# Optimization experiments

Hardware: AMD Instinct MI355X
Metric: run time of the kernel (lower is better)

## Reference

```python
import jax, jax.numpy as jnp
import numpy as np

TWO_PI = 6.283185  # constant used verbatim in the original module


def setup_inputs() -> dict:
    key = jax.random.key(0)
    ks = jax.random.split(key, 12)
    N, input_size, light_freq, H = 8388608, 11, 16, 16
    d_in = input_size - 2 + 2 * light_freq  # 41
    x = jax.random.uniform(ks[0], (N, input_size), dtype=jnp.float32)
    B_light = jax.random.normal(ks[1], (2, light_freq), dtype=jnp.float32)
    W1 = jax.random.normal(ks[2], (d_in, H), dtype=jnp.float32) * (1.0 / np.sqrt(d_in))
    b1 = jax.random.normal(ks[3], (H,), dtype=jnp.float32) * 0.01
    W2 = jax.random.normal(ks[4], (H, H), dtype=jnp.float32) * 0.25
    b2 = jax.random.normal(ks[5], (H,), dtype=jnp.float32) * 0.01
    W3 = jax.random.normal(ks[6], (H, H), dtype=jnp.float32) * 0.25
    b3 = jax.random.normal(ks[7], (H,), dtype=jnp.float32) * 0.01
    W4 = jax.random.normal(ks[8], (H, H), dtype=jnp.float32) * 0.25
    b4 = jax.random.normal(ks[9], (H,), dtype=jnp.float32) * 0.01
    W5 = jax.random.normal(ks[10], (H, 1), dtype=jnp.float32) * 0.25
    b5 = jax.random.normal(ks[11], (1,), dtype=jnp.float32) * 0.01
    return {"x": x, "B_light": B_light, "W1": W1, "b1": b1, "W2": W2, "b2": b2,
            "W3": W3, "b3": b3, "W4": W4, "b4": b4, "W5": W5, "b5": b5}


def reference(x, B_light, W1, b1, W2, b2, W3, b3, W4, b4, W5, b5):
    # Fourier-feature encoding of the last two input dims (light direction)
    x_light = TWO_PI * (x[:, -2:] @ B_light)                      # [N, F]
    feats = jnp.concatenate([x[:, :-2], jnp.cos(x_light), jnp.sin(x_light)], axis=-1)  # [N, 41]
    # Tiny 5-layer MLP with ELU activations
    h = jax.nn.elu(feats @ W1 + b1)
    h = jax.nn.elu(h @ W2 + b2)
    h = jax.nn.elu(h @ W3 + b3)
    h = jax.nn.elu(h @ W4 + b4)
    out = h @ W5 + b5                                             # [N, 1]
    return out
```

## Files before the change

kernel.cpp:

```cpp
#include <hip/hip_runtime.h>

typedef __fp16   cvt16x2 __attribute__((ext_vector_type(2)));
typedef _Float16 h2      __attribute__((ext_vector_type(2)));
typedef _Float16 half4_t __attribute__((ext_vector_type(4)));
typedef unsigned uint2v  __attribute__((ext_vector_type(2)));
typedef float    f32x4   __attribute__((ext_vector_type(4)));
typedef float    f32x4u  __attribute__((ext_vector_type(4), aligned(4)));

#define CH 8
#define LOG2E 1.44269504f
#define LN2   0.69314718f

#if !__has_builtin(__builtin_elementwise_exp2)
extern "C" __device__ _Float16 __ocml_exp2_f16(_Float16);
#endif

__device__ __forceinline__ unsigned pk(float a, float b) {
    cvt16x2 h = __builtin_amdgcn_cvt_pkrtz(a, b);
    return __builtin_bit_cast(unsigned, h);
}
__device__ __forceinline__ half4_t mkfrag(unsigned lo, unsigned hi) {
    uint2v u; u[0] = lo; u[1] = hi;
    return __builtin_bit_cast(half4_t, u);
}

__device__ __forceinline__ unsigned elu_pk(float a, float b) {
    h2 v = __builtin_bit_cast(h2, __builtin_amdgcn_cvt_pkrtz(a, b));
    const h2 z   = {(_Float16)0.f, (_Float16)0.f};
    const h2 lg  = {(_Float16)LOG2E, (_Float16)LOG2E};
    const h2 mlg = {(_Float16)(-LOG2E), (_Float16)(-LOG2E)};
    h2 t = __builtin_elementwise_min(v, z);
#if __has_builtin(__builtin_elementwise_exp2)
    h2 ev = __builtin_elementwise_exp2(t);
#else
    h2 ev; ev[0] = __ocml_exp2_f16(t[0]); ev[1] = __ocml_exp2_f16(t[1]);
#endif
    h2 r = __builtin_elementwise_max(v, ev * lg + mlg);
    return __builtin_bit_cast(unsigned, r);
}

__global__ __launch_bounds__(128, 4) void pixenc_mfma14(
    const float* __restrict__ x,
    const float* __restrict__ Bl,
    const float* __restrict__ W1, const float* __restrict__ b1,
    const float* __restrict__ W2, const float* __restrict__ b2,
    const float* __restrict__ W3, const float* __restrict__ b3,
    const float* __restrict__ W4, const float* __restrict__ b4,
    const float* __restrict__ W5, const float* __restrict__ b5,
    float* __restrict__ out)
{
    const int t    = threadIdx.x;
    const int lane = t & 63;
    const int w    = t >> 6;
    const int g    = lane >> 4;
    const int m    = lane & 15;

    const int coff = (g == 0) ? 7 : (g == 2) ? 3 : 0;

    half4_t A1[3], A2, A3, A4;
    #pragma unroll
    for (int e = 0; e < 4; ++e) {
        const bool valid = (g == 1) | (g == 0 && e < 2) | (g == 2 && e >= 1);
        A1[0][e] = valid ? (_Float16)(W1[(coff + e) * 16 + m] * LOG2E)
                         : (_Float16)0.f;
        A1[1][e] = (_Float16)(W1[(9  + g * 4 + e) * 16 + m] * LOG2E);
        A1[2][e] = (_Float16)(W1[(25 + g * 4 + e) * 16 + m] * LOG2E);
        A2[e]    = (_Float16)W2[(g * 4 + e) * 16 + m];
        A3[e]    = (_Float16)W3[(g * 4 + e) * 16 + m];
        A4[e]    = (_Float16)W4[(g * 4 + e) * 16 + m];
    }
    const half4_t Az = (g == 0) ? mkfrag(pk(Bl[m], Bl[16 + m]), 0u)
                                : mkfrag(0u, 0u);
    const half4_t A5 = (m == 0)
        ? mkfrag(pk(W5[g * 4 + 0] * LN2, W5[g * 4 + 1] * LN2),
                 pk(W5[g * 4 + 2] * LN2, W5[g * 4 + 3] * LN2))
        : mkfrag(0u, 0u);
    f32x4 c1, c2, c3, c4;
    #pragma unroll
    for (int e = 0; e < 4; ++e) {
        const int r = g * 4 + e;
        c1[e] = b1[r] * LOG2E; c2[e] = b2[r] * LOG2E;
        c3[e] = b3[r] * LOG2E; c4[e] = b4[r] * LOG2E;
    }
    const f32x4 zero4 = {0.f, 0.f, 0.f, 0.f};
    f32x4 c5 = zero4;
    if (g == 0) c5[0] = b5[0];

    const int wavebase = blockIdx.x * (128 * CH) + w * (64 * CH);
    const float* aP = x + (size_t)(wavebase + m) * 11 + coff;
    float* outp = out + wavebase + m;

    unsigned cp01[4], cp23[4];
    #pragma unroll
    for (int s = 0; s < 4; ++s) {
        const f32x4u v = *(const f32x4u*)(aP + s * 176);
        cp01[s] = pk(v[0], v[1]);
        cp23[s] = pk(v[2], v[3]);
    }

    #pragma unroll
    for (int c = 0; c < CH; ++c) {
        unsigned np01[4], np23[4];
        if (c + 1 < CH) {
            aP += 704;
            #pragma unroll
            for (int s = 0; s < 4; ++s) {
                const f32x4u v = *(const f32x4u*)(aP + s * 176);
                np01[s] = pk(v[0], v[1]);
                np23[s] = pk(v[2], v[3]);
            }
        }

        f32x4 az[4];
        #pragma unroll
        for (int s = 0; s < 4; ++s)
            az[s] = __builtin_amdgcn_mfma_f32_16x16x16f16(
                        Az, mkfrag(cp23[s], 0u), zero4, 0, 0, 0);

        f32x4 acc[4];
        #pragma unroll
        for (int s = 0; s < 4; ++s) {
            float cs[4], sn[4];
            #pragma unroll
            for (int e = 0; e < 4; ++e) {
                cs[e] = __builtin_amdgcn_cosf(az[s][e]);
                sn[e] = __builtin_amdgcn_sinf(az[s][e]);
            }
            const half4_t F0 = mkfrag(cp01[s], cp23[s]);
            const half4_t F1 = mkfrag(pk(cs[0], cs[1]), pk(cs[2], cs[3]));
            const half4_t F2 = mkfrag(pk(sn[0], sn[1]), pk(sn[2], sn[3]));
            f32x4 a = __builtin_amdgcn_mfma_f32_16x16x16f16(A1[0], F0, c1, 0, 0, 0);
            a = __builtin_amdgcn_mfma_f32_16x16x16f16(A1[1], F1, a, 0, 0, 0);
            a = __builtin_amdgcn_mfma_f32_16x16x16f16(A1[2], F2, a, 0, 0, 0);
            acc[s] = a;
        }

        half4_t H[4];
        #pragma unroll
        for (int s = 0; s < 4; ++s)
            H[s] = mkfrag(elu_pk(acc[s][0], acc[s][1]), elu_pk(acc[s][2], acc[s][3]));
        #pragma unroll
        for (int s = 0; s < 4; ++s)
            acc[s] = __builtin_amdgcn_mfma_f32_16x16x16f16(A2, H[s], c2, 0, 0, 0);

        #pragma unroll
        for (int s = 0; s < 4; ++s)
            H[s] = mkfrag(elu_pk(acc[s][0], acc[s][1]), elu_pk(acc[s][2], acc[s][3]));
        #pragma unroll
        for (int s = 0; s < 4; ++s)
            acc[s] = __builtin_amdgcn_mfma_f32_16x16x16f16(A3, H[s], c3, 0, 0, 0);

        #pragma unroll
        for (int s = 0; s < 4; ++s)
            H[s] = mkfrag(elu_pk(acc[s][0], acc[s][1]), elu_pk(acc[s][2], acc[s][3]));
        #pragma unroll
        for (int s = 0; s < 4; ++s)
            acc[s] = __builtin_amdgcn_mfma_f32_16x16x16f16(A4, H[s], c4, 0, 0, 0);

        #pragma unroll
        for (int s = 0; s < 4; ++s)
            H[s] = mkfrag(elu_pk(acc[s][0], acc[s][1]), elu_pk(acc[s][2], acc[s][3]));
        #pragma unroll
        for (int s = 0; s < 4; ++s) {
            const f32x4 oh = __builtin_amdgcn_mfma_f32_16x16x16f16(
                                 A5, H[s], c5, 0, 0, 0);
            if (g == 0) outp[c * 64 + s * 16] = oh[0];
        }

        if (c + 1 < CH) {
            #pragma unroll
            for (int s = 0; s < 4; ++s) {
                cp01[s] = np01[s]; cp23[s] = np23[s];
            }
        }
    }
}

__global__ void pixenc_tail(
    const float* __restrict__ x, const float* __restrict__ Bl,
    const float* __restrict__ W1, const float* __restrict__ b1,
    const float* __restrict__ W2, const float* __restrict__ b2,
    const float* __restrict__ W3, const float* __restrict__ b3,
    const float* __restrict__ W4, const float* __restrict__ b4,
    const float* __restrict__ W5, const float* __restrict__ b5,
    float* __restrict__ out, int N, int start)
{
    const int i = start + blockIdx.x * 256 + threadIdx.x;
    if (i >= N) return;
    const float* xr = x + (size_t)i * 11;
    float feats[41];
    for (int k = 0; k < 9; ++k) feats[k] = xr[k];
    for (int f = 0; f < 16; ++f) {
        const float ang = 6.283185f * (xr[9] * Bl[f] + xr[10] * Bl[16 + f]);
        float s, c; __sincosf(ang, &s, &c);
        feats[9 + f] = c; feats[25 + f] = s;
    }
    float h[16], gg[16];
    for (int j = 0; j < 16; ++j) h[j] = b1[j];
    for (int k = 0; k < 41; ++k)
        for (int j = 0; j < 16; ++j) h[j] = fmaf(feats[k], W1[k * 16 + j], h[j]);
    for (int j = 0; j < 16; ++j) h[j] = h[j] > 0.f ? h[j] : __expf(h[j]) - 1.f;
    for (int j = 0; j < 16; ++j) gg[j] = b2[j];
    for (int k = 0; k < 16; ++k)
        for (int j = 0; j < 16; ++j) gg[j] = fmaf(h[k], W2[k * 16 + j], gg[j]);
    for (int j = 0; j < 16; ++j) gg[j] = gg[j] > 0.f ? gg[j] : __expf(gg[j]) - 1.f;
    for (int j = 0; j < 16; ++j) h[j] = b3[j];
    for (int k = 0; k < 16; ++k)
        for (int j = 0; j < 16; ++j) h[j] = fmaf(gg[k], W3[k * 16 + j], h[j]);
    for (int j = 0; j < 16; ++j) h[j] = h[j] > 0.f ? h[j] : __expf(h[j]) - 1.f;
    for (int j = 0; j < 16; ++j) gg[j] = b4[j];
    for (int k = 0; k < 16; ++k)
        for (int j = 0; j < 16; ++j) gg[j] = fmaf(h[k], W4[k * 16 + j], gg[j]);
    for (int j = 0; j < 16; ++j) gg[j] = gg[j] > 0.f ? gg[j] : __expf(gg[j]) - 1.f;
    float o = b5[0];
    for (int j = 0; j < 16; ++j) o = fmaf(gg[j], W5[j], o);
    out[i] = o;
}

extern "C" void kernel_launch(void* const* d_in, const int* in_sizes, int n_in,
                              void* d_out, int out_size, void* d_ws, size_t ws_size,
                              hipStream_t stream) {
    const float* x  = (const float*)d_in[0];
    const float* Bl = (const float*)d_in[1];
    const float* W1 = (const float*)d_in[2];
    const float* b1 = (const float*)d_in[3];
    const float* W2 = (const float*)d_in[4];
    const float* b2 = (const float*)d_in[5];
    const float* W3 = (const float*)d_in[6];
    const float* b3 = (const float*)d_in[7];
    const float* W4 = (const float*)d_in[8];
    const float* b4 = (const float*)d_in[9];
    const float* W5 = (const float*)d_in[10];
    const float* b5 = (const float*)d_in[11];
    float* out = (float*)d_out;

    const int N = out_size;
    const int NB = N / (128 * CH);
    const int rem = N - NB * (128 * CH);
    if (NB > 0)
        pixenc_mfma14<<<NB, 128, 0, stream>>>(x, Bl, W1, b1, W2, b2, W3, b3,
                                              W4, b4, W5, b5, out);
    if (rem > 0)
        pixenc_tail<<<(rem + 255) / 256, 256, 0, stream>>>(
            x, Bl, W1, b1, W2, b2, W3, b3, W4, b4, W5, b5, out, N, NB * 128 * CH);
}
```

Before: 120.4 us.

## Process one 16-sample tile per iteration to cut registers and raise occupancy

Each wave now handles one 16-sample MFMA tile per loop iteration instead of four interleaved tiles, unrolled by two, with single-tile prefetch of the next input row. Launch bounds move to 8 waves per SIMD and the bias b5 is added as a scalar after the last MFMA. The aim is lower VGPR pressure and higher occupancy, hiding latency through more resident waves rather than instruction-level parallelism within a wave. The trade-off is less independent MFMA and transcendental work per wave to overlap dependent chains.

```diff
diff --git a/kernel.cpp b/kernel.cpp
--- a/kernel.cpp
+++ b/kernel.cpp
@@ -7,7 +7,7 @@
 typedef float    f32x4   __attribute__((ext_vector_type(4)));
 typedef float    f32x4u  __attribute__((ext_vector_type(4), aligned(4)));
 
-#define CH 8
+#define NSB 32
 #define LOG2E 1.44269504f
 #define LN2   0.69314718f
 
@@ -39,7 +39,7 @@
     return __builtin_bit_cast(unsigned, r);
 }
 
-__global__ __launch_bounds__(128, 4) void pixenc_mfma14(
+__global__ __launch_bounds__(128, 8) void pixenc_mfma17(
     const float* __restrict__ x,
     const float* __restrict__ Bl,
     const float* __restrict__ W1, const float* __restrict__ b1,
@@ -83,96 +83,55 @@
         c3[e] = b3[r] * LOG2E; c4[e] = b4[r] * LOG2E;
     }
     const f32x4 zero4 = {0.f, 0.f, 0.f, 0.f};
-    f32x4 c5 = zero4;
-    if (g == 0) c5[0] = b5[0];
-
-    const int wavebase = blockIdx.x * (128 * CH) + w * (64 * CH);
+    const float b5v = b5[0];
+
+    const int wavebase = blockIdx.x * (32 * NSB) + w * (16 * NSB);
     const float* aP = x + (size_t)(wavebase + m) * 11 + coff;
     float* outp = out + wavebase + m;
 
-    unsigned cp01[4], cp23[4];
-    #pragma unroll
-    for (int s = 0; s < 4; ++s) {
-        const f32x4u v = *(const f32x4u*)(aP + s * 176);
-        cp01[s] = pk(v[0], v[1]);
-        cp23[s] = pk(v[2], v[3]);
-    }
-
-    #pragma unroll
-    for (int c = 0; c < CH; ++c) {
-        unsigned np01[4], np23[4];
-        if (c + 1 < CH) {
-            aP += 704;
-            #pragma unroll
-            for (int s = 0; s < 4; ++s) {
-                const f32x4u v = *(const f32x4u*)(aP + s * 176);
-                np01[s] = pk(v[0], v[1]);
-                np23[s] = pk(v[2], v[3]);
-            }
+    unsigned cp01, cp23;
+    {
+        const f32x4u v = *(const f32x4u*)aP;
+        cp01 = pk(v[0], v[1]);
+        cp23 = pk(v[2], v[3]);
+    }
+
+    #pragma unroll 2
+    for (int it = 0; it < NSB; ++it) {
+        unsigned np01, np23;
+        if (it + 1 < NSB) {
+            const f32x4u v = *(const f32x4u*)(aP + 176);
+            np01 = pk(v[0], v[1]);
+            np23 = pk(v[2], v[3]);
         }
-
-        f32x4 az[4];
+        aP += 176;
+
+        const f32x4 az = __builtin_amdgcn_mfma_f32_16x16x16f16(
+                             Az, mkfrag(cp23, 0u), zero4, 0, 0, 0);
+        float cs[4], sn[4];
         #pragma unroll
-        for (int s = 0; s < 4; ++s)
-            az[s] = __builtin_amdgcn_mfma_f32_16x16x16f16(
-                        Az, mkfrag(cp23[s], 0u), zero4, 0, 0, 0);
-
-        f32x4 acc[4];
-        #pragma unroll
-        for (int s = 0; s < 4; ++s) {
-            float cs[4], sn[4];
-            #pragma unroll
-            for (int e = 0; e < 4; ++e) {
-                cs[e] = __builtin_amdgcn_cosf(az[s][e]);
-                sn[e] = __builtin_amdgcn_sinf(az[s][e]);
-            }
-            const half4_t F0 = mkfrag(cp01[s], cp23[s]);
-            const half4_t F1 = mkfrag(pk(cs[0], cs[1]), pk(cs[2], cs[3]));
-            const half4_t F2 = mkfrag(pk(sn[0], sn[1]), pk(sn[2], sn[3]));
-            f32x4 a = __builtin_amdgcn_mfma_f32_16x16x16f16(A1[0], F0, c1, 0, 0, 0);
-            a = __builtin_amdgcn_mfma_f32_16x16x16f16(A1[1], F1, a, 0, 0, 0);
-            a = __builtin_amdgcn_mfma_f32_16x16x16f16(A1[2], F2, a, 0, 0, 0);
-            acc[s] = a;
+        for (int e = 0; e < 4; ++e) {
+            cs[e] = __builtin_amdgcn_cosf(az[e]);
+            sn[e] = __builtin_amdgcn_sinf(az[e]);
         }
-
-        half4_t H[4];
-        #pragma unroll
-        for (int s = 0; s < 4; ++s)
-            H[s] = mkfrag(elu_pk(acc[s][0], acc[s][1]), elu_pk(acc[s][2], acc[s][3]));
-        #pragma unroll
-        for (int s = 0; s < 4; ++s)
-            acc[s] = __builtin_amdgcn_mfma_f32_16x16x16f16(A2, H[s], c2, 0, 0, 0);
-
-        #pragma unroll
-        for (int s = 0; s < 4; ++s)
-            H[s] = mkfrag(elu_pk(acc[s][0], acc[s][1]), elu_pk(acc[s][2], acc[s][3]));
-        #pragma unroll
-        for (int s = 0; s < 4; ++s)
-            acc[s] = __builtin_amdgcn_mfma_f32_16x16x16f16(A3, H[s], c3, 0, 0, 0);
-
-        #pragma unroll
-        for (int s = 0; s < 4; ++s)
-            H[s] = mkfrag(elu_pk(acc[s][0], acc[s][1]), elu_pk(acc[s][2], acc[s][3]));
-        #pragma unroll
-        for (int s = 0; s < 4; ++s)
-            acc[s] = __builtin_amdgcn_mfma_f32_16x16x16f16(A4, H[s], c4, 0, 0, 0);
-
-        #pragma unroll
-        for (int s = 0; s < 4; ++s)
-            H[s] = mkfrag(elu_pk(acc[s][0], acc[s][1]), elu_pk(acc[s][2], acc[s][3]));
-        #pragma unroll
-        for (int s = 0; s < 4; ++s) {
-            const f32x4 oh = __builtin_amdgcn_mfma_f32_16x16x16f16(
-                                 A5, H[s], c5, 0, 0, 0);
-            if (g == 0) outp[c * 64 + s * 16] = oh[0];
-        }
-
-        if (c + 1 < CH) {
-            #pragma unroll
-            for (int s = 0; s < 4; ++s) {
-                cp01[s] = np01[s]; cp23[s] = np23[s];
-            }
-        }
+        const half4_t F0 = mkfrag(cp01, cp23);
+        const half4_t F1 = mkfrag(pk(cs[0], cs[1]), pk(cs[2], cs[3]));
+        const half4_t F2 = mkfrag(pk(sn[0], sn[1]), pk(sn[2], sn[3]));
+        f32x4 a = __builtin_amdgcn_mfma_f32_16x16x16f16(A1[0], F0, c1, 0, 0, 0);
+        a = __builtin_amdgcn_mfma_f32_16x16x16f16(A1[1], F1, a, 0, 0, 0);
+        a = __builtin_amdgcn_mfma_f32_16x16x16f16(A1[2], F2, a, 0, 0, 0);
+
+        a = __builtin_amdgcn_mfma_f32_16x16x16f16(
+                A2, mkfrag(elu_pk(a[0], a[1]), elu_pk(a[2], a[3])), c2, 0, 0, 0);
+        a = __builtin_amdgcn_mfma_f32_16x16x16f16(
+                A3, mkfrag(elu_pk(a[0], a[1]), elu_pk(a[2], a[3])), c3, 0, 0, 0);
+        a = __builtin_amdgcn_mfma_f32_16x16x16f16(
+                A4, mkfrag(elu_pk(a[0], a[1]), elu_pk(a[2], a[3])), c4, 0, 0, 0);
+        const f32x4 oh = __builtin_amdgcn_mfma_f32_16x16x16f16(
+                A5, mkfrag(elu_pk(a[0], a[1]), elu_pk(a[2], a[3])), zero4, 0, 0, 0);
+        if (g == 0) outp[it * 16] = oh[0] + b5v;
+
+        if (it + 1 < NSB) { cp01 = np01; cp23 = np23; }
     }
 }
 
@@ -235,12 +194,14 @@
     float* out = (float*)d_out;
 
     const int N = out_size;
-    const int NB = N / (128 * CH);
-    const int rem = N - NB * (128 * CH);
+    const int samples_per_block = 32 * NSB;
+    const int NB = N / samples_per_block;
+    const int rem = N - NB * samples_per_block;
     if (NB > 0)
-        pixenc_mfma14<<<NB, 128, 0, stream>>>(x, Bl, W1, b1, W2, b2, W3, b3,
+        pixenc_mfma17<<<NB, 128, 0, stream>>>(x, Bl, W1, b1, W2, b2, W3, b3,
                                               W4, b4, W5, b5, out);
     if (rem > 0)
         pixenc_tail<<<(rem + 255) / 256, 256, 0, stream>>>(
-            x, Bl, W1, b1, W2, b2, W3, b3, W4, b4, W5, b5, out, N, NB * 128 * CH);
-}
+            x, Bl, W1, b1, W2, b2, W3, b3, W4, b4, W5, b5, out, N,
+            NB * samples_per_block);
+}
```

New measurement: 125.1 us. 3.9% more time.
